# Kernel tuning notes

Hardware: AMD Instinct MI355X
Metric: run time of the kernel (lower is better)

Reference implementation:

```python
import jax, jax.numpy as jnp
import numpy as np

N = 50000
E = 500000
IN_DIM = 384
HID = 128
HEADS = 4
OUT_DIM = 384
NEG_SLOPE = 0.2


def gat_conv(x, edge_index, W, att_src, att_dst, bias):
    """PyG GATConv (concat=True, add_self_loops=True, eval mode).
    x: [N, F_in]; edge_index: [2, E] (row 0 = source j, row 1 = target i);
    W: [F_in, H*C]; att_src/att_dst: [H, C]; bias: [H*C].
    """
    n = x.shape[0]
    # add self loops
    loops = jnp.arange(n, dtype=edge_index.dtype)
    src = jnp.concatenate([edge_index[0], loops])
    dst = jnp.concatenate([edge_index[1], loops])

    h = (x @ W).reshape(n, HEADS, -1)              # [N, H, C]
    a_src = jnp.einsum('nhc,hc->nh', h, att_src)   # [N, H]
    a_dst = jnp.einsum('nhc,hc->nh', h, att_dst)   # [N, H]

    e = a_src[src] + a_dst[dst]                    # [E', H]
    e = jax.nn.leaky_relu(e, NEG_SLOPE)
    # segment softmax over incoming edges of each target node
    e_max = jax.ops.segment_max(e, dst, num_segments=n)
    e_exp = jnp.exp(e - e_max[dst])
    denom = jax.ops.segment_sum(e_exp, dst, num_segments=n)
    alpha = e_exp / denom[dst]                     # [E', H]

    msg = h[src] * alpha[:, :, None]               # [E', H, C]
    out = jax.ops.segment_sum(msg, dst, num_segments=n)  # [N, H, C]
    return out.reshape(n, -1) + bias


def setup_inputs() -> dict:
    key = jax.random.key(0)
    ks = jax.random.split(key, 12)
    s_in = 1.0 / np.sqrt(IN_DIM)
    s_h = 1.0 / np.sqrt(HEADS * HID)
    return {
        'x': jax.random.normal(ks[0], (N, IN_DIM), dtype=jnp.float32),
        'edge_index': jax.random.randint(ks[1], (2, E), 0, N, dtype=jnp.int32),
        'W1': jax.random.normal(ks[2], (IN_DIM, HEADS * HID), dtype=jnp.float32) * s_in,
        'a1_src': jax.random.normal(ks[3], (HEADS, HID), dtype=jnp.float32) * s_in,
        'a1_dst': jax.random.normal(ks[4], (HEADS, HID), dtype=jnp.float32) * s_in,
        'b1': jnp.zeros((HEADS * HID,), dtype=jnp.float32),
        'W2': jax.random.normal(ks[5], (HEADS * HID, HEADS * HID), dtype=jnp.float32) * s_h,
        'a2_src': jax.random.normal(ks[6], (HEADS, HID), dtype=jnp.float32) * s_h,
        'a2_dst': jax.random.normal(ks[7], (HEADS, HID), dtype=jnp.float32) * s_h,
        'b2': jnp.zeros((HEADS * HID,), dtype=jnp.float32),
        'Wfc': jax.random.normal(ks[8], (HEADS * HID, OUT_DIM), dtype=jnp.float32) * s_h,
        'bfc': jnp.zeros((OUT_DIM,), dtype=jnp.float32),
    }


def reference(x, edge_index, W1, a1_src, a1_dst, b1, W2, a2_src, a2_dst, b2, Wfc, bfc):
    h = jax.nn.relu(gat_conv(x, edge_index, W1, a1_src, a1_dst, b1))
    h = jax.nn.relu(gat_conv(h, edge_index, W2, a2_src, a2_dst, b2))
    return h @ Wfc + bfc  # [N, OUT_DIM]
```

## Files before the change

### kernel.cpp

```cpp
#include <hip/hip_runtime.h>
#include <cfloat>
#include <cstdint>

#define HEADS 4
#define HIDC 128
#define HC 512
#define NEG 0.2f

typedef _Float16 half8 __attribute__((ext_vector_type(8)));
typedef float floatx4 __attribute__((ext_vector_type(4)));

__global__ __launch_bounds__(256) void mfma_gemm(
    const _Float16* __restrict__ A,
    const _Float16* __restrict__ Bt,
    _Float16* __restrict__ Ch,
    float* __restrict__ Cf,
    const float* __restrict__ bias,
    const float* __restrict__ atts,
    const float* __restrict__ attd,
    float* __restrict__ a_src,
    float* __restrict__ a_dst,
    int M, int N, int K)
{
    __shared__ __align__(16) _Float16 As[128 * 64];
    __shared__ __align__(16) _Float16 Bs[128 * 64];

    const int nwg = gridDim.x * gridDim.y;
    int lin = blockIdx.y * gridDim.x + blockIdx.x;
    {
        const int q = nwg >> 3, r = nwg & 7;
        const int xcd = lin & 7, pos = lin >> 3;
        lin = (xcd < r ? xcd * (q + 1) : r * (q + 1) + (xcd - r) * q) + pos;
    }
    const int bx = lin % gridDim.x;
    const int by = lin / gridDim.x;

    const int tid = threadIdx.x;
    const int w = tid >> 6;
    const int lane = tid & 63;
    const int wr = (w >> 1) * 64;
    const int wc = (w & 1) * 64;

    const int rowBase = by * 128;
    const int colBase = bx * 128;

    const int strow = lane >> 3;
    const int sColSw = (((lane & 7) ^ strow) * 8);

    floatx4 acc[4][4];
#pragma unroll
    for (int i = 0; i < 4; i++)
#pragma unroll
        for (int j = 0; j < 4; j++) acc[i][j] = {0.f, 0.f, 0.f, 0.f};

    const int q16 = lane >> 4;
    const int l16 = lane & 15;

    for (int k0 = 0; k0 < K; k0 += 64) {
#pragma unroll
        for (int c = 0; c < 4; c++) {
            const int rr = (c * 4 + w) * 8;
            const _Float16* ga = A + (size_t)(rowBase + rr + strow) * K + k0 + sColSw;
            const _Float16* gb = Bt + (size_t)(colBase + rr + strow) * K + k0 + sColSw;
            __builtin_amdgcn_global_load_lds(
                (const __attribute__((address_space(1))) unsigned int*)ga,
                (__attribute__((address_space(3))) unsigned int*)&As[rr * 64], 16, 0, 0);
            __builtin_amdgcn_global_load_lds(
                (const __attribute__((address_space(1))) unsigned int*)gb,
                (__attribute__((address_space(3))) unsigned int*)&Bs[rr * 64], 16, 0, 0);
        }
        __syncthreads();

#pragma unroll
        for (int s = 0; s < 2; s++) {
            half8 af[4], bf[4];
#pragma unroll
            for (int i = 0; i < 4; i++) {
                const int r = wr + i * 16 + l16;
                af[i] = *(const half8*)&As[r * 64 + (((s * 4 + q16) ^ (r & 7)) * 8)];
            }
#pragma unroll
            for (int j = 0; j < 4; j++) {
                const int r = wc + j * 16 + l16;
                bf[j] = *(const half8*)&Bs[r * 64 + (((s * 4 + q16) ^ (r & 7)) * 8)];
            }
#pragma unroll
            for (int i = 0; i < 4; i++)
#pragma unroll
                for (int j = 0; j < 4; j++)
                    acc[i][j] = __builtin_amdgcn_mfma_f32_16x16x32_f16(af[i], bf[j], acc[i][j], 0, 0, 0);
        }
        __syncthreads();
    }

    if (Ch) {
#pragma unroll
        for (int i = 0; i < 4; i++)
#pragma unroll
            for (int j = 0; j < 4; j++) {
                const int col = colBase + wc + j * 16 + l16;
#pragma unroll
                for (int r = 0; r < 4; r++) {
                    const int row = rowBase + wr + i * 16 + q16 * 4 + r;
                    if (row < M) Ch[(size_t)row * N + col] = (_Float16)acc[i][j][r];
                }
            }
    }
    if (Cf) {
#pragma unroll
        for (int i = 0; i < 4; i++)
#pragma unroll
            for (int j = 0; j < 4; j++) {
                const int col = colBase + wc + j * 16 + l16;
                const float bb = bias ? bias[col] : 0.f;
#pragma unroll
                for (int r = 0; r < 4; r++) {
                    const int row = rowBase + wr + i * 16 + q16 * 4 + r;
                    if (row < M) Cf[(size_t)row * N + col] = acc[i][j][r] + bb;
                }
            }
    }

    if (atts) {
        float* ps = (float*)As;
        float* pd = ps + 256;
        const int head = bx;
        float as[4], ad[4];
#pragma unroll
        for (int j = 0; j < 4; j++) {
            const int cl = wc + j * 16 + l16;
            as[j] = atts[head * HIDC + cl];
            ad[j] = attd[head * HIDC + cl];
        }
#pragma unroll
        for (int i = 0; i < 4; i++) {
#pragma unroll
            for (int r = 0; r < 4; r++) {
                float s_ = acc[i][0][r] * as[0] + acc[i][1][r] * as[1]
                         + acc[i][2][r] * as[2] + acc[i][3][r] * as[3];
                float d_ = acc[i][0][r] * ad[0] + acc[i][1][r] * ad[1]
                         + acc[i][2][r] * ad[2] + acc[i][3][r] * ad[3];
#pragma unroll
                for (int mk = 1; mk <= 8; mk <<= 1) {
                    s_ += __shfl_xor(s_, mk);
                    d_ += __shfl_xor(d_, mk);
                }
                if (l16 == 0) {
                    const int rloc = wr + i * 16 + q16 * 4 + r;
                    ps[(wc >> 6) * 128 + rloc] = s_;
                    pd[(wc >> 6) * 128 + rloc] = d_;
                }
            }
        }
        __syncthreads();
        if (tid < 128) {
            const int row = rowBase + tid;
            if (row < M) {
                a_src[(size_t)row * 4 + head] = ps[tid] + ps[128 + tid];
                a_dst[(size_t)row * 4 + head] = pd[tid] + pd[128 + tid];
            }
        }
    }
}

__global__ void convert_x_kernel(const float* __restrict__ x, _Float16* __restrict__ o, size_t nquads)
{
    size_t i = (size_t)blockIdx.x * blockDim.x + threadIdx.x;
    if (i < nquads) {
        float4 v = *(const float4*)(x + i * 4);
        _Float16* p = o + i * 4;
        p[0] = (_Float16)v.x; p[1] = (_Float16)v.y;
        p[2] = (_Float16)v.z; p[3] = (_Float16)v.w;
    }
}

__global__ void convert_wT3_kernel(
    const float* __restrict__ W1, const float* __restrict__ W2, const float* __restrict__ W3,
    _Float16* __restrict__ T1, _Float16* __restrict__ T2, _Float16* __restrict__ T3)
{
    const int z = blockIdx.z;
    const float* W = (z == 0) ? W1 : (z == 1) ? W2 : W3;
    _Float16* T = (z == 0) ? T1 : (z == 1) ? T2 : T3;
    const int K = (z == 0) ? 384 : 512;
    const int N = (z == 2) ? 384 : 512;
    int k = blockIdx.x * 64 + (threadIdx.x & 63);
    int n = blockIdx.y * 4 + (threadIdx.x >> 6);
    if (k < K && n < N) T[(size_t)n * K + k] = (_Float16)W[(size_t)k * N + n];
}

__global__ void count_kernel(const int* __restrict__ dst, int* __restrict__ deg, int E)
{
    int e = blockIdx.x * blockDim.x + threadIdx.x;
    if (e < E) atomicAdd(&deg[dst[e]], 1);
}

__global__ __launch_bounds__(256) void block_sum_kernel(
    const int* __restrict__ deg, int* __restrict__ bsum, int Nn)
{
    int gid = blockIdx.x * 256 + threadIdx.x;
    int v = (gid < Nn) ? deg[gid] : 0;
#pragma unroll
    for (int o = 32; o >= 1; o >>= 1) v += __shfl_xor(v, o);
    __shared__ int ws[4];
    if ((threadIdx.x & 63) == 0) ws[threadIdx.x >> 6] = v;
    __syncthreads();
    if (threadIdx.x == 0) bsum[blockIdx.x] = ws[0] + ws[1] + ws[2] + ws[3];
}

__global__ __launch_bounds__(256) void scan_bsum_kernel(
    const int* __restrict__ bsum, int* __restrict__ bbase, int nb)
{
    __shared__ int s[256];
    const int tid = threadIdx.x;
    int v = (tid < nb) ? bsum[tid] : 0;
    s[tid] = v;
    __syncthreads();
    for (int off = 1; off < 256; off <<= 1) {
        int t = (tid >= off) ? s[tid - off] : 0;
        __syncthreads();
        s[tid] += t;
        __syncthreads();
    }
    if (tid < nb) bbase[tid] = s[tid] - v;
}

__global__ __launch_bounds__(256) void fill_rowptr_kernel(
    const int* __restrict__ deg, const int* __restrict__ bbase,
    int* __restrict__ rowptr, int* __restrict__ cursor, int Nn, int E)
{
    __shared__ int s[256];
    const int tid = threadIdx.x;
    const int gid = blockIdx.x * 256 + tid;
    int v = (gid < Nn) ? deg[gid] : 0;
    s[tid] = v;
    __syncthreads();
    for (int off = 1; off < 256; off <<= 1) {
        int t = (tid >= off) ? s[tid - off] : 0;
        __syncthreads();
        s[tid] += t;
        __syncthreads();
    }
    if (gid < Nn) {
        int r = bbase[blockIdx.x] + s[tid] - v;
        rowptr[gid] = r;
        cursor[gid] = r;
    }
    if (gid == 0) rowptr[Nn] = E;
}

__global__ void fill_kernel(const int* __restrict__ src, const int* __restrict__ dst,
                            int* __restrict__ cursor, int* __restrict__ eidx, int E)
{
    int e = blockIdx.x * blockDim.x + threadIdx.x;
    if (e < E) {
        int d = dst[e];
        int pos = atomicAdd(&cursor[d], 1);
        eidx[pos] = src[e];
    }
}

__global__ __launch_bounds__(128) void gather_kernel(
    const _Float16* __restrict__ h, const float* __restrict__ a_src,
    const float* __restrict__ a_dst,
    const int* __restrict__ rowptr, const int* __restrict__ eidx,
    const float* __restrict__ bias, _Float16* __restrict__ out, int Nn)
{
    const int wv = __builtin_amdgcn_readfirstlane(threadIdx.x >> 6);
    const int node = blockIdx.x * 2 + wv;
    if (node >= Nn) return;
    const int lane = threadIdx.x & 63;
    const int hd = lane >> 4;

    const int beg = rowptr[node];
    const int deg = rowptr[node + 1] - beg;
    const int total = deg + 1;

    const float ad = a_dst[(size_t)node * 4 + hd];
    const _Float16* hb = h + (size_t)lane * 8;

    float acc[8];
#pragma unroll
    for (int i = 0; i < 8; i++) acc[i] = 0.f;
    float dsum = 0.f;

    for (int base = 0; base < total; base += 64) {
        const int cnt = min(total - base, 64);
        const int t = base + lane;
        int myIdx = node;
        if (t < deg) myIdx = eidx[beg + t];

        for (int e = 0; e < cnt; e += 4) {
            const int s0 = __shfl(myIdx, e);
            const int s1 = __shfl(myIdx, e + 1);
            const int s2 = __shfl(myIdx, e + 2);
            const int s3 = __shfl(myIdx, e + 3);
            half8 hv0 = *(const half8*)(hb + (size_t)s0 * HC);
            half8 hv1 = *(const half8*)(hb + (size_t)s1 * HC);
            half8 hv2 = *(const half8*)(hb + (size_t)s2 * HC);
            half8 hv3 = *(const half8*)(hb + (size_t)s3 * HC);
            const float as0 = a_src[(size_t)s0 * 4 + hd];
            const float as1 = a_src[(size_t)s1 * 4 + hd];
            const float as2 = a_src[(size_t)s2 * 4 + hd];
            const float as3 = a_src[(size_t)s3 * 4 + hd];
            float l0 = as0 + ad; l0 = l0 > 0.f ? l0 : NEG * l0;
            float l1 = as1 + ad; l1 = l1 > 0.f ? l1 : NEG * l1;
            float l2 = as2 + ad; l2 = l2 > 0.f ? l2 : NEG * l2;
            float l3 = as3 + ad; l3 = l3 > 0.f ? l3 : NEG * l3;
            const float w0 = __expf(l0);
            const float w1 = (e + 1 < cnt) ? __expf(l1) : 0.f;
            const float w2 = (e + 2 < cnt) ? __expf(l2) : 0.f;
            const float w3 = (e + 3 < cnt) ? __expf(l3) : 0.f;
            dsum += (w0 + w1) + (w2 + w3);
#pragma unroll
            for (int i = 0; i < 8; i++)
                acc[i] += (w0 * (float)hv0[i] + w1 * (float)hv1[i])
                        + (w2 * (float)hv2[i] + w3 * (float)hv3[i]);
        }
    }

    const float is = 1.f / dsum;
    const float* bp = bias + lane * 8;
    half8 ov;
#pragma unroll
    for (int i = 0; i < 8; i++) {
        float o = acc[i] * is + bp[i];
        o = o > 0.f ? o : 0.f;
        ov[i] = (_Float16)o;
    }
    *(half8*)(out + (size_t)node * HC + (size_t)lane * 8) = ov;
}

extern "C" void kernel_launch(void* const* d_in, const int* in_sizes, int n_in,
                              void* d_out, int out_size, void* d_ws, size_t ws_size,
                              hipStream_t stream)
{
    const float* x   = (const float*)d_in[0];
    const int*   ei  = (const int*)d_in[1];
    const float* W1  = (const float*)d_in[2];
    const float* a1s = (const float*)d_in[3];
    const float* a1d = (const float*)d_in[4];
    const float* b1  = (const float*)d_in[5];
    const float* W2  = (const float*)d_in[6];
    const float* a2s = (const float*)d_in[7];
    const float* a2d = (const float*)d_in[8];
    const float* b2  = (const float*)d_in[9];
    const float* Wfc = (const float*)d_in[10];
    const float* bfc = (const float*)d_in[11];
    float* out = (float*)d_out;

    const int Nn  = in_sizes[0] / 384;
    const int E   = in_sizes[1] / 2;
    const int IN  = 384;
    const int OUT = in_sizes[11];
    const int Mp  = ((Nn + 127) / 128) * 128;
    const int nb  = (Nn + 255) / 256;

    uint8_t* p = (uint8_t*)d_ws;
    auto alloc = [&](size_t bytes) {
        uint8_t* r = p;
        p += (bytes + 255) & ~(size_t)255;
        return r;
    };
    _Float16* Ah_x = (_Float16*)alloc((size_t)Mp * IN * 2);
    _Float16* Ah_g = (_Float16*)alloc((size_t)Mp * HC * 2);
    _Float16* Hh   = (_Float16*)alloc((size_t)Mp * HC * 2);
    _Float16* Wt1  = (_Float16*)alloc((size_t)HC * IN * 2);
    _Float16* Wt2  = (_Float16*)alloc((size_t)HC * HC * 2);
    _Float16* Wt3  = (_Float16*)alloc((size_t)OUT * HC * 2);
    float* a_src   = (float*)alloc((size_t)Nn * 4 * 4);
    float* a_dst   = (float*)alloc((size_t)Nn * 4 * 4);
    int* deg       = (int*)alloc((size_t)Nn * 4);
    int* rowptr    = (int*)alloc((size_t)(Nn + 1) * 4);
    int* cursor    = (int*)alloc((size_t)Nn * 4);
    int* eidx      = (int*)alloc((size_t)E * 4);
    int* bsum      = (int*)alloc((size_t)nb * 4);
    int* bbase     = (int*)alloc((size_t)nb * 4);

    const int* e_src = ei;
    const int* e_dst = ei + E;

    {
        size_t nq = (size_t)Nn * IN / 4;
        convert_x_kernel<<<(nq + 255) / 256, 256, 0, stream>>>(x, Ah_x, nq);
        dim3 gw(8, 128, 3);
        convert_wT3_kernel<<<gw, 256, 0, stream>>>(W1, W2, Wfc, Wt1, Wt2, Wt3);
    }

    hipMemsetAsync(deg, 0, Nn * sizeof(int), stream);
    const int eb = (E + 255) / 256;
    count_kernel<<<eb, 256, 0, stream>>>(e_dst, deg, E);
    block_sum_kernel<<<nb, 256, 0, stream>>>(deg, bsum, Nn);
    scan_bsum_kernel<<<1, 256, 0, stream>>>(bsum, bbase, nb);
    fill_rowptr_kernel<<<nb, 256, 0, stream>>>(deg, bbase, rowptr, cursor, Nn, E);
    fill_kernel<<<eb, 256, 0, stream>>>(e_src, e_dst, cursor, eidx, E);

    const dim3 gg1(HC / 128, Mp / 128);
    const int gb = (Nn + 1) / 2;

    mfma_gemm<<<gg1, 256, 0, stream>>>(Ah_x, Wt1, Hh, nullptr, nullptr,
                                       a1s, a1d, a_src, a_dst, Nn, HC, IN);
    gather_kernel<<<gb, 128, 0, stream>>>(Hh, a_src, a_dst, rowptr, eidx, b1, Ah_g, Nn);

    mfma_gemm<<<gg1, 256, 0, stream>>>(Ah_g, Wt2, Hh, nullptr, nullptr,
                                       a2s, a2d, a_src, a_dst, Nn, HC, HC);
    gather_kernel<<<gb, 128, 0, stream>>>(Hh, a_src, a_dst, rowptr, eidx, b2, Ah_g, Nn);

    const dim3 gg3(OUT / 128, Mp / 128);
    mfma_gemm<<<gg3, 256, 0, stream>>>(Ah_g, Wt3, nullptr, out, bfc,
                                       nullptr, nullptr, nullptr, nullptr, Nn, OUT, HC);
}
```

Before: 536.8 us.

## Store features column-blocked and precompute edge weights for per-block gather

The GEMM output H and the gather output are now stored in 32-column blocks (one Mp×32 slab per block), and the GEMM reads A in that layout when Acb is set. A new edge_weight kernel computes the exp(leaky_relu) attention weights once per edge and per self loop, using a destination array written during CSR fill. The gather kernel is restructured so each block handles one 32-column slab for 64 nodes, with 4 lanes per node and a software-prefetched edge loop. The intent is to improve cache locality of the random row gathers by shrinking the working set per slab and to remove the redundant per-lane attention math. The cost is an extra kernel launch and extra weight traffic per layer, plus lane imbalance because each 16-node wave loops to its maximum degree.

```diff
diff --git a/kernel.cpp b/kernel.cpp
--- a/kernel.cpp
+++ b/kernel.cpp
@@ -20,7 +20,7 @@
     const float* __restrict__ attd,
     float* __restrict__ a_src,
     float* __restrict__ a_dst,
-    int M, int N, int K)
+    int M, int N, int K, int Acb)
 {
     __shared__ __align__(16) _Float16 As[128 * 64];
     __shared__ __align__(16) _Float16 Bs[128 * 64];
@@ -44,8 +44,27 @@
     const int rowBase = by * 128;
     const int colBase = bx * 128;
 
+    const size_t Mp32 = (size_t)gridDim.y * 128 * 32;
+
     const int strow = lane >> 3;
-    const int sColSw = (((lane & 7) ^ strow) * 8);
+    const int sColSw = ((lane & 7) ^ strow) * 8;
+
+    const _Float16* gaP[4];
+    const _Float16* gbP[4];
+    _Float16* lA[4];
+    _Float16* lB[4];
+#pragma unroll
+    for (int c = 0; c < 4; c++) {
+        const int rr = c * 32 + w * 8;
+        const int rA = rowBase + rr + strow;
+        const int rB = colBase + rr + strow;
+        gaP[c] = Acb ? (A + (size_t)(sColSw >> 5) * Mp32 + (size_t)rA * 32 + (sColSw & 31))
+                     : (A + (size_t)rA * K + sColSw);
+        gbP[c] = Bt + (size_t)rB * K + sColSw;
+        lA[c] = &As[rr * 64];
+        lB[c] = &Bs[rr * 64];
+    }
+    const size_t kA = Acb ? (Mp32 * 2) : (size_t)64;
 
     floatx4 acc[4][4];
 #pragma unroll
@@ -59,15 +78,14 @@
     for (int k0 = 0; k0 < K; k0 += 64) {
 #pragma unroll
         for (int c = 0; c < 4; c++) {
-            const int rr = (c * 4 + w) * 8;
-            const _Float16* ga = A + (size_t)(rowBase + rr + strow) * K + k0 + sColSw;
-            const _Float16* gb = Bt + (size_t)(colBase + rr + strow) * K + k0 + sColSw;
             __builtin_amdgcn_global_load_lds(
-                (const __attribute__((address_space(1))) unsigned int*)ga,
-                (__attribute__((address_space(3))) unsigned int*)&As[rr * 64], 16, 0, 0);
+                (const __attribute__((address_space(1))) unsigned int*)gaP[c],
+                (__attribute__((address_space(3))) unsigned int*)lA[c], 16, 0, 0);
             __builtin_amdgcn_global_load_lds(
-                (const __attribute__((address_space(1))) unsigned int*)gb,
-                (__attribute__((address_space(3))) unsigned int*)&Bs[rr * 64], 16, 0, 0);
+                (const __attribute__((address_space(1))) unsigned int*)gbP[c],
+                (__attribute__((address_space(3))) unsigned int*)lB[c], 16, 0, 0);
+            gaP[c] += kA;
+            gbP[c] += 64;
         }
         __syncthreads();
 
@@ -99,10 +117,11 @@
 #pragma unroll
             for (int j = 0; j < 4; j++) {
                 const int col = colBase + wc + j * 16 + l16;
+                const size_t cbase = (size_t)(col >> 5) * Mp32 + (col & 31);
 #pragma unroll
                 for (int r = 0; r < 4; r++) {
                     const int row = rowBase + wr + i * 16 + q16 * 4 + r;
-                    if (row < M) Ch[(size_t)row * N + col] = (_Float16)acc[i][j][r];
+                    if (row < M) Ch[cbase + (size_t)row * 32] = (_Float16)acc[i][j][r];
                 }
             }
     }
@@ -249,85 +268,132 @@
 }
 
 __global__ void fill_kernel(const int* __restrict__ src, const int* __restrict__ dst,
-                            int* __restrict__ cursor, int* __restrict__ eidx, int E)
+                            int* __restrict__ cursor, int* __restrict__ eidx,
+                            int* __restrict__ edst, int E)
 {
     int e = blockIdx.x * blockDim.x + threadIdx.x;
     if (e < E) {
         int d = dst[e];
         int pos = atomicAdd(&cursor[d], 1);
         eidx[pos] = src[e];
-    }
-}
-
-__global__ __launch_bounds__(128) void gather_kernel(
-    const _Float16* __restrict__ h, const float* __restrict__ a_src,
-    const float* __restrict__ a_dst,
+        edst[pos] = d;
+    }
+}
+
+__global__ __launch_bounds__(256) void edge_weight_kernel(
+    const int* __restrict__ eidx, const int* __restrict__ edst,
+    const float* __restrict__ a_src, const float* __restrict__ a_dst,
+    float* __restrict__ wH, float* __restrict__ wS, int E, int Ep, int Nn)
+{
+    int p = blockIdx.x * 256 + threadIdx.x;
+    if (p < E) {
+        int s = eidx[p];
+        int d = edst[p];
+        float4 as4 = *(const float4*)(a_src + (size_t)s * 4);
+        float4 ad4 = *(const float4*)(a_dst + (size_t)d * 4);
+        float l0 = as4.x + ad4.x; l0 = l0 > 0.f ? l0 : NEG * l0;
+        float l1 = as4.y + ad4.y; l1 = l1 > 0.f ? l1 : NEG * l1;
+        float l2 = as4.z + ad4.z; l2 = l2 > 0.f ? l2 : NEG * l2;
+        float l3 = as4.w + ad4.w; l3 = l3 > 0.f ? l3 : NEG * l3;
+        wH[0 * Ep + p] = __expf(l0);
+        wH[1 * Ep + p] = __expf(l1);
+        wH[2 * Ep + p] = __expf(l2);
+        wH[3 * Ep + p] = __expf(l3);
+    } else if (p < E + Nn) {
+        int n = p - E;
+        float4 as4 = *(const float4*)(a_src + (size_t)n * 4);
+        float4 ad4 = *(const float4*)(a_dst + (size_t)n * 4);
+        float l0 = as4.x + ad4.x; l0 = l0 > 0.f ? l0 : NEG * l0;
+        float l1 = as4.y + ad4.y; l1 = l1 > 0.f ? l1 : NEG * l1;
+        float l2 = as4.z + ad4.z; l2 = l2 > 0.f ? l2 : NEG * l2;
+        float l3 = as4.w + ad4.w; l3 = l3 > 0.f ? l3 : NEG * l3;
+        wS[0 * Nn + n] = __expf(l0);
+        wS[1 * Nn + n] = __expf(l1);
+        wS[2 * Nn + n] = __expf(l2);
+        wS[3 * Nn + n] = __expf(l3);
+    }
+}
+
+__global__ __launch_bounds__(256) void gather_kernel(
+    const _Float16* __restrict__ h,
+    const float* __restrict__ wH,
+    const float* __restrict__ wS,
     const int* __restrict__ rowptr, const int* __restrict__ eidx,
-    const float* __restrict__ bias, _Float16* __restrict__ out, int Nn)
-{
-    const int wv = __builtin_amdgcn_readfirstlane(threadIdx.x >> 6);
-    const int node = blockIdx.x * 2 + wv;
-    if (node >= Nn) return;
-    const int lane = threadIdx.x & 63;
-    const int hd = lane >> 4;
-
-    const int beg = rowptr[node];
-    const int deg = rowptr[node + 1] - beg;
-    const int total = deg + 1;
-
-    const float ad = a_dst[(size_t)node * 4 + hd];
-    const _Float16* hb = h + (size_t)lane * 8;
+    const float* __restrict__ bias, _Float16* __restrict__ out,
+    int Nn, int Mp, int Ep, int nchunks)
+{
+    const int half = nchunks << 3;
+    int lin = blockIdx.x;
+    int cb;
+    if (lin < half) { cb = lin & 7; }
+    else { lin -= half; cb = 8 + (lin & 7); }
+    const int chunk = lin >> 3;
+
+    const int tid = threadIdx.x;
+    const int wv = tid >> 6;
+    const int lane = tid & 63;
+    const int g = lane >> 2;
+    const int l4 = lane & 3;
+    const int node = chunk * 64 + wv * 16 + g;
+    const bool valid = node < Nn;
+
+    const int hd = cb >> 2;
+    const size_t Mp32 = (size_t)Mp * 32;
+    const _Float16* hs = h + (size_t)cb * Mp32 + l4 * 8;
+    const float* wHp = wH + (size_t)hd * Ep;
+
+    int beg = 0, deg = 0;
+    float wSv = 0.f;
+    if (valid) {
+        beg = rowptr[node];
+        deg = rowptr[node + 1] - beg;
+        wSv = wS[(size_t)hd * Nn + node];
+    }
+
+    int mx = valid ? deg + 1 : 0;
+#pragma unroll
+    for (int m = 4; m <= 32; m <<= 1) {
+        int o = __shfl_xor(mx, m);
+        mx = o > mx ? o : mx;
+    }
 
     float acc[8];
 #pragma unroll
     for (int i = 0; i < 8; i++) acc[i] = 0.f;
     float dsum = 0.f;
 
-    for (int base = 0; base < total; base += 64) {
-        const int cnt = min(total - base, 64);
-        const int t = base + lane;
-        int myIdx = node;
-        if (t < deg) myIdx = eidx[beg + t];
-
-        for (int e = 0; e < cnt; e += 4) {
-            const int s0 = __shfl(myIdx, e);
-            const int s1 = __shfl(myIdx, e + 1);
-            const int s2 = __shfl(myIdx, e + 2);
-            const int s3 = __shfl(myIdx, e + 3);
-            half8 hv0 = *(const half8*)(hb + (size_t)s0 * HC);
-            half8 hv1 = *(const half8*)(hb + (size_t)s1 * HC);
-            half8 hv2 = *(const half8*)(hb + (size_t)s2 * HC);
-            half8 hv3 = *(const half8*)(hb + (size_t)s3 * HC);
-            const float as0 = a_src[(size_t)s0 * 4 + hd];
-            const float as1 = a_src[(size_t)s1 * 4 + hd];
-            const float as2 = a_src[(size_t)s2 * 4 + hd];
-            const float as3 = a_src[(size_t)s3 * 4 + hd];
-            float l0 = as0 + ad; l0 = l0 > 0.f ? l0 : NEG * l0;
-            float l1 = as1 + ad; l1 = l1 > 0.f ? l1 : NEG * l1;
-            float l2 = as2 + ad; l2 = l2 > 0.f ? l2 : NEG * l2;
-            float l3 = as3 + ad; l3 = l3 > 0.f ? l3 : NEG * l3;
-            const float w0 = __expf(l0);
-            const float w1 = (e + 1 < cnt) ? __expf(l1) : 0.f;
-            const float w2 = (e + 2 < cnt) ? __expf(l2) : 0.f;
-            const float w3 = (e + 3 < cnt) ? __expf(l3) : 0.f;
-            dsum += (w0 + w1) + (w2 + w3);
-#pragma unroll
-            for (int i = 0; i < 8; i++)
-                acc[i] += (w0 * (float)hv0[i] + w1 * (float)hv1[i])
-                        + (w2 * (float)hv2[i] + w3 * (float)hv3[i]);
-        }
-    }
-
-    const float is = 1.f / dsum;
-    const float* bp = bias + lane * 8;
-    half8 ov;
-#pragma unroll
-    for (int i = 0; i < 8; i++) {
-        float o = acc[i] * is + bp[i];
-        o = o > 0.f ? o : 0.f;
-        ov[i] = (_Float16)o;
-    }
-    *(half8*)(out + (size_t)node * HC + (size_t)lane * 8) = ov;
+    int sC = node;
+    float wC = 0.f;
+    if (0 < deg)      { sC = eidx[beg]; wC = wHp[beg]; }
+    else if (0 == deg && valid) wC = wSv;
+
+    for (int e = 0; e < mx; e++) {
+        half8 hv = *(const half8*)(hs + (size_t)sC * 32);
+        const float wf = wC;
+        int sN = node;
+        float wN = 0.f;
+        const int en = e + 1;
+        if (en < deg)       { sN = eidx[beg + en]; wN = wHp[beg + en]; }
+        else if (en == deg && valid) wN = wSv;
+        sC = sN; wC = wN;
+
+        dsum += wf;
+#pragma unroll
+        for (int i = 0; i < 8; i++) acc[i] += wf * (float)hv[i];
+    }
+
+    if (valid) {
+        const float is = 1.f / dsum;
+        const float* bp = bias + cb * 32 + l4 * 8;
+        half8 ov;
+#pragma unroll
+        for (int i = 0; i < 8; i++) {
+            float o = acc[i] * is + bp[i];
+            o = o > 0.f ? o : 0.f;
+            ov[i] = (_Float16)o;
+        }
+        *(half8*)(out + (size_t)cb * Mp32 + (size_t)node * 32 + l4 * 8) = ov;
+    }
 }
 
 extern "C" void kernel_launch(void* const* d_in, const int* in_sizes, int n_in,
@@ -354,6 +420,7 @@
     const int OUT = in_sizes[11];
     const int Mp  = ((Nn + 127) / 128) * 128;
     const int nb  = (Nn + 255) / 256;
+    const int Ep  = E + 16;
 
     uint8_t* p = (uint8_t*)d_ws;
     auto alloc = [&](size_t bytes) {
@@ -372,7 +439,10 @@
     int* deg       = (int*)alloc((size_t)Nn * 4);
     int* rowptr    = (int*)alloc((size_t)(Nn + 1) * 4);
     int* cursor    = (int*)alloc((size_t)Nn * 4);
-    int* eidx      = (int*)alloc((size_t)E * 4);
+    int* eidx      = (int*)alloc((size_t)Ep * 4);
+    int* edst      = (int*)alloc((size_t)E * 4);
+    float* wH      = (float*)alloc((size_t)4 * Ep * 4);
+    float* wS      = (float*)alloc((size_t)4 * Nn * 4);
     int* bsum      = (int*)alloc((size_t)nb * 4);
     int* bbase     = (int*)alloc((size_t)nb * 4);
 
@@ -392,20 +462,26 @@
     block_sum_kernel<<<nb, 256, 0, stream>>>(deg, bsum, Nn);
     scan_bsum_kernel<<<1, 256, 0, stream>>>(bsum, bbase, nb);
     fill_rowptr_kernel<<<nb, 256, 0, stream>>>(deg, bbase, rowptr, cursor, Nn, E);
-    fill_kernel<<<eb, 256, 0, stream>>>(e_src, e_dst, cursor, eidx, E);
+    fill_kernel<<<eb, 256, 0, stream>>>(e_src, e_dst, cursor, eidx, edst, E);
 
     const dim3 gg1(HC / 128, Mp / 128);
-    const int gb = (Nn + 1) / 2;
+    const int nchunks = (Nn + 63) / 64;
+    const int gwb = 16 * nchunks;
+    const int ewb = (E + Nn + 255) / 256;
 
     mfma_gemm<<<gg1, 256, 0, stream>>>(Ah_x, Wt1, Hh, nullptr, nullptr,
-                                       a1s, a1d, a_src, a_dst, Nn, HC, IN);
-    gather_kernel<<<gb, 128, 0, stream>>>(Hh, a_src, a_dst, rowptr, eidx, b1, Ah_g, Nn);
+                                       a1s, a1d, a_src, a_dst, Nn, HC, IN, 0);
+    edge_weight_kernel<<<ewb, 256, 0, stream>>>(eidx, edst, a_src, a_dst, wH, wS, E, Ep, Nn);
+    gather_kernel<<<gwb, 256, 0, stream>>>(Hh, wH, wS, rowptr, eidx, b1, Ah_g,
+                                           Nn, Mp, Ep, nchunks);
 
     mfma_gemm<<<gg1, 256, 0, stream>>>(Ah_g, Wt2, Hh, nullptr, nullptr,
-                                       a2s, a2d, a_src, a_dst, Nn, HC, HC);
-    gather_kernel<<<gb, 128, 0, stream>>>(Hh, a_src, a_dst, rowptr, eidx, b2, Ah_g, Nn);
+                                       a2s, a2d, a_src, a_dst, Nn, HC, HC, 1);
+    edge_weight_kernel<<<ewb, 256, 0, stream>>>(eidx, edst, a_src, a_dst, wH, wS, E, Ep, Nn);
+    gather_kernel<<<gwb, 256, 0, stream>>>(Hh, wH, wS, rowptr, eidx, b2, Ah_g,
+                                           Nn, Mp, Ep, nchunks);
 
     const dim3 gg3(OUT / 128, Mp / 128);
     mfma_gemm<<<gg3, 256, 0, stream>>>(Ah_g, Wt3, nullptr, out, bfc,
-                                       nullptr, nullptr, nullptr, nullptr, Nn, OUT, HC);
-}
+                                       nullptr, nullptr, nullptr, nullptr, Nn, OUT, HC, 1);
+}
```

After: 559.5 us. 4.2% more time.

## Use persistent atomic work-queue gather and hoist GEMM load address math

Applied to the files above, without the earlier changes.

The gather kernel becomes persistent: 2048 blocks of 4 wavefronts each pull node indices from a global atomic counter. The counter is reset inside the scan kernel. The per-edge loop now reads eidx directly with 2-way unrolling instead of broadcasting indices through shuffles, and the bias is hoisted out of the node loop. The GEMM precomputes its global and LDS load pointers once and bumps them per k-step, and it uses nontemporal stores for outputs, as does the gather. The aim is to balance irregular degrees and cut per-block launch overhead, at the cost of one atomic per node and less memory-level parallelism per edge iteration.

```diff
diff --git a/kernel.cpp b/kernel.cpp
--- a/kernel.cpp
+++ b/kernel.cpp
@@ -9,6 +9,7 @@
 
 typedef _Float16 half8 __attribute__((ext_vector_type(8)));
 typedef float floatx4 __attribute__((ext_vector_type(4)));
+typedef unsigned int uint4v __attribute__((ext_vector_type(4)));
 
 __global__ __launch_bounds__(256) void mfma_gemm(
     const _Float16* __restrict__ A,
@@ -45,7 +46,20 @@
     const int colBase = bx * 128;
 
     const int strow = lane >> 3;
-    const int sColSw = (((lane & 7) ^ strow) * 8);
+    const int sColSw = ((lane & 7) ^ strow) * 8;
+
+    const _Float16* gaP[4];
+    const _Float16* gbP[4];
+    _Float16* lA[4];
+    _Float16* lB[4];
+#pragma unroll
+    for (int c = 0; c < 4; c++) {
+        const int rr = c * 32 + w * 8;
+        gaP[c] = A + (size_t)(rowBase + rr + strow) * K + sColSw;
+        gbP[c] = Bt + (size_t)(colBase + rr + strow) * K + sColSw;
+        lA[c] = &As[rr * 64];
+        lB[c] = &Bs[rr * 64];
+    }
 
     floatx4 acc[4][4];
 #pragma unroll
@@ -59,15 +73,14 @@
     for (int k0 = 0; k0 < K; k0 += 64) {
 #pragma unroll
         for (int c = 0; c < 4; c++) {
-            const int rr = (c * 4 + w) * 8;
-            const _Float16* ga = A + (size_t)(rowBase + rr + strow) * K + k0 + sColSw;
-            const _Float16* gb = Bt + (size_t)(colBase + rr + strow) * K + k0 + sColSw;
             __builtin_amdgcn_global_load_lds(
-                (const __attribute__((address_space(1))) unsigned int*)ga,
-                (__attribute__((address_space(3))) unsigned int*)&As[rr * 64], 16, 0, 0);
+                (const __attribute__((address_space(1))) unsigned int*)gaP[c],
+                (__attribute__((address_space(3))) unsigned int*)lA[c], 16, 0, 0);
             __builtin_amdgcn_global_load_lds(
-                (const __attribute__((address_space(1))) unsigned int*)gb,
-                (__attribute__((address_space(3))) unsigned int*)&Bs[rr * 64], 16, 0, 0);
+                (const __attribute__((address_space(1))) unsigned int*)gbP[c],
+                (__attribute__((address_space(3))) unsigned int*)lB[c], 16, 0, 0);
+            gaP[c] += 64;
+            gbP[c] += 64;
         }
         __syncthreads();
 
@@ -102,7 +115,9 @@
 #pragma unroll
                 for (int r = 0; r < 4; r++) {
                     const int row = rowBase + wr + i * 16 + q16 * 4 + r;
-                    if (row < M) Ch[(size_t)row * N + col] = (_Float16)acc[i][j][r];
+                    if (row < M)
+                        __builtin_nontemporal_store((_Float16)acc[i][j][r],
+                                                    &Ch[(size_t)row * N + col]);
                 }
             }
     }
@@ -116,7 +131,9 @@
 #pragma unroll
                 for (int r = 0; r < 4; r++) {
                     const int row = rowBase + wr + i * 16 + q16 * 4 + r;
-                    if (row < M) Cf[(size_t)row * N + col] = acc[i][j][r] + bb;
+                    if (row < M)
+                        __builtin_nontemporal_store(acc[i][j][r] + bb,
+                                                    &Cf[(size_t)row * N + col]);
                 }
             }
     }
@@ -208,7 +225,7 @@
 }
 
 __global__ __launch_bounds__(256) void scan_bsum_kernel(
-    const int* __restrict__ bsum, int* __restrict__ bbase, int nb)
+    const int* __restrict__ bsum, int* __restrict__ bbase, int* __restrict__ ctr, int nb)
 {
     __shared__ int s[256];
     const int tid = threadIdx.x;
@@ -222,6 +239,7 @@
         __syncthreads();
     }
     if (tid < nb) bbase[tid] = s[tid] - v;
+    if (tid < 2) ctr[tid] = 0;
 }
 
 __global__ __launch_bounds__(256) void fill_rowptr_kernel(
@@ -259,75 +277,90 @@
     }
 }
 
-__global__ __launch_bounds__(128) void gather_kernel(
+__global__ __launch_bounds__(256) void gather_kernel(
     const _Float16* __restrict__ h, const float* __restrict__ a_src,
     const float* __restrict__ a_dst,
     const int* __restrict__ rowptr, const int* __restrict__ eidx,
-    const float* __restrict__ bias, _Float16* __restrict__ out, int Nn)
-{
-    const int wv = __builtin_amdgcn_readfirstlane(threadIdx.x >> 6);
-    const int node = blockIdx.x * 2 + wv;
-    if (node >= Nn) return;
+    const float* __restrict__ bias, _Float16* __restrict__ out,
+    int* __restrict__ ctr, int Nn)
+{
     const int lane = threadIdx.x & 63;
     const int hd = lane >> 4;
-
-    const int beg = rowptr[node];
-    const int deg = rowptr[node + 1] - beg;
-    const int total = deg + 1;
-
-    const float ad = a_dst[(size_t)node * 4 + hd];
     const _Float16* hb = h + (size_t)lane * 8;
 
-    float acc[8];
-#pragma unroll
-    for (int i = 0; i < 8; i++) acc[i] = 0.f;
-    float dsum = 0.f;
-
-    for (int base = 0; base < total; base += 64) {
-        const int cnt = min(total - base, 64);
-        const int t = base + lane;
-        int myIdx = node;
-        if (t < deg) myIdx = eidx[beg + t];
-
-        for (int e = 0; e < cnt; e += 4) {
-            const int s0 = __shfl(myIdx, e);
-            const int s1 = __shfl(myIdx, e + 1);
-            const int s2 = __shfl(myIdx, e + 2);
-            const int s3 = __shfl(myIdx, e + 3);
+    float bv[8];
+    {
+        const float* bp = bias + lane * 8;
+#pragma unroll
+        for (int i = 0; i < 8; i++) bv[i] = bp[i];
+    }
+
+    for (;;) {
+        int node;
+        if (lane == 0) node = atomicAdd(ctr, 1);
+        node = __shfl(node, 0);
+        if (node >= Nn) break;
+
+        const int beg = rowptr[node];
+        const int deg = rowptr[node + 1] - beg;
+
+        const float ad = a_dst[(size_t)node * 4 + hd];
+
+        float acc[8];
+#pragma unroll
+        for (int i = 0; i < 8; i++) acc[i] = 0.f;
+        float dsum = 0.f;
+
+        {
+            const float as = a_src[(size_t)node * 4 + hd];
+            half8 hv = *(const half8*)(hb + (size_t)node * HC);
+            float l = as + ad; l = l > 0.f ? l : NEG * l;
+            const float w = __expf(l);
+            dsum += w;
+#pragma unroll
+            for (int i = 0; i < 8; i++) acc[i] += w * (float)hv[i];
+        }
+
+        int e = 0;
+        for (; e + 2 <= deg; e += 2) {
+            const int s0 = eidx[beg + e];
+            const int s1 = eidx[beg + e + 1];
             half8 hv0 = *(const half8*)(hb + (size_t)s0 * HC);
             half8 hv1 = *(const half8*)(hb + (size_t)s1 * HC);
-            half8 hv2 = *(const half8*)(hb + (size_t)s2 * HC);
-            half8 hv3 = *(const half8*)(hb + (size_t)s3 * HC);
             const float as0 = a_src[(size_t)s0 * 4 + hd];
             const float as1 = a_src[(size_t)s1 * 4 + hd];
-            const float as2 = a_src[(size_t)s2 * 4 + hd];
-            const float as3 = a_src[(size_t)s3 * 4 + hd];
             float l0 = as0 + ad; l0 = l0 > 0.f ? l0 : NEG * l0;
             float l1 = as1 + ad; l1 = l1 > 0.f ? l1 : NEG * l1;
-            float l2 = as2 + ad; l2 = l2 > 0.f ? l2 : NEG * l2;
-            float l3 = as3 + ad; l3 = l3 > 0.f ? l3 : NEG * l3;
             const float w0 = __expf(l0);
-            const float w1 = (e + 1 < cnt) ? __expf(l1) : 0.f;
-            const float w2 = (e + 2 < cnt) ? __expf(l2) : 0.f;
-            const float w3 = (e + 3 < cnt) ? __expf(l3) : 0.f;
-            dsum += (w0 + w1) + (w2 + w3);
-#pragma unroll
-            for (int i = 0; i < 8; i++)
-                acc[i] += (w0 * (float)hv0[i] + w1 * (float)hv1[i])
-                        + (w2 * (float)hv2[i] + w3 * (float)hv3[i]);
-        }
-    }
-
-    const float is = 1.f / dsum;
-    const float* bp = bias + lane * 8;
-    half8 ov;
-#pragma unroll
-    for (int i = 0; i < 8; i++) {
-        float o = acc[i] * is + bp[i];
-        o = o > 0.f ? o : 0.f;
-        ov[i] = (_Float16)o;
-    }
-    *(half8*)(out + (size_t)node * HC + (size_t)lane * 8) = ov;
+            const float w1 = __expf(l1);
+            dsum += w0 + w1;
+#pragma unroll
+            for (int i = 0; i < 8; i++) acc[i] += w0 * (float)hv0[i];
+#pragma unroll
+            for (int i = 0; i < 8; i++) acc[i] += w1 * (float)hv1[i];
+        }
+        if (e < deg) {
+            const int s0 = eidx[beg + e];
+            half8 hv0 = *(const half8*)(hb + (size_t)s0 * HC);
+            const float as0 = a_src[(size_t)s0 * 4 + hd];
+            float l0 = as0 + ad; l0 = l0 > 0.f ? l0 : NEG * l0;
+            const float w0 = __expf(l0);
+            dsum += w0;
+#pragma unroll
+            for (int i = 0; i < 8; i++) acc[i] += w0 * (float)hv0[i];
+        }
+
+        const float is = 1.f / dsum;
+        half8 ov;
+#pragma unroll
+        for (int i = 0; i < 8; i++) {
+            float o = acc[i] * is + bv[i];
+            o = o > 0.f ? o : 0.f;
+            ov[i] = (_Float16)o;
+        }
+        uint4v uv = *(uint4v*)&ov;
+        __builtin_nontemporal_store(uv, (uint4v*)(out + (size_t)node * HC + (size_t)lane * 8));
+    }
 }
 
 extern "C" void kernel_launch(void* const* d_in, const int* in_sizes, int n_in,
@@ -375,6 +408,7 @@
     int* eidx      = (int*)alloc((size_t)E * 4);
     int* bsum      = (int*)alloc((size_t)nb * 4);
     int* bbase     = (int*)alloc((size_t)nb * 4);
+    int* ctr       = (int*)alloc(2 * 4);
 
     const int* e_src = ei;
     const int* e_dst = ei + E;
@@ -386,24 +420,26 @@
         convert_wT3_kernel<<<gw, 256, 0, stream>>>(W1, W2, Wfc, Wt1, Wt2, Wt3);
     }
 
-    hipMemsetAsync(deg, 0, Nn * sizeof(int), stream);
+    (void)hipMemsetAsync(deg, 0, Nn * sizeof(int), stream);
     const int eb = (E + 255) / 256;
     count_kernel<<<eb, 256, 0, stream>>>(e_dst, deg, E);
     block_sum_kernel<<<nb, 256, 0, stream>>>(deg, bsum, Nn);
-    scan_bsum_kernel<<<1, 256, 0, stream>>>(bsum, bbase, nb);
+    scan_bsum_kernel<<<1, 256, 0, stream>>>(bsum, bbase, ctr, nb);
     fill_rowptr_kernel<<<nb, 256, 0, stream>>>(deg, bbase, rowptr, cursor, Nn, E);
     fill_kernel<<<eb, 256, 0, stream>>>(e_src, e_dst, cursor, eidx, E);
 
     const dim3 gg1(HC / 128, Mp / 128);
-    const int gb = (Nn + 1) / 2;
+    const int gb = 2048;
 
     mfma_gemm<<<gg1, 256, 0, stream>>>(Ah_x, Wt1, Hh, nullptr, nullptr,
                                        a1s, a1d, a_src, a_dst, Nn, HC, IN);
-    gather_kernel<<<gb, 128, 0, stream>>>(Hh, a_src, a_dst, rowptr, eidx, b1, Ah_g, Nn);
+    gather_kernel<<<gb, 256, 0, stream>>>(Hh, a_src, a_dst, rowptr, eidx, b1, Ah_g,
+                                          ctr + 0, Nn);
 
     mfma_gemm<<<gg1, 256, 0, stream>>>(Ah_g, Wt2, Hh, nullptr, nullptr,
                                        a2s, a2d, a_src, a_dst, Nn, HC, HC);
-    gather_kernel<<<gb, 128, 0, stream>>>(Hh, a_src, a_dst, rowptr, eidx, b2, Ah_g, Nn);
+    gather_kernel<<<gb, 256, 0, stream>>>(Hh, a_src, a_dst, rowptr, eidx, b2, Ah_g,
+                                          ctr + 1, Nn);
 
     const dim3 gg3(OUT / 128, Mp / 128);
     mfma_gemm<<<gg3, 256, 0, stream>>>(Ah_g, Wt3, nullptr, out, bfc,
```

New measurement: 1.746 ms. 225% more time.
